# Kernel optimization log

Hardware: AMD Instinct MI355X
Metric: run time of the kernel (lower is better)

## Reference

```python
import jax, jax.numpy as jnp
import numpy as np

N_E = 1024
E_DIM = 256
BETA = 0.25
EPS_MASK = 1e-6
EPS_LOG = 1e-10


def setup_inputs() -> dict:
    key = jax.random.key(0)
    k1, k2, k3 = jax.random.split(key, 3)
    z = jax.random.normal(k1, (128, 512, E_DIM), dtype=jnp.float32)
    mask = jax.random.randint(k2, (128, 512), 0, 2, dtype=jnp.int32)
    emb_w = jax.random.uniform(k3, (N_E, E_DIM), dtype=jnp.float32,
                               minval=-1.0 / N_E, maxval=1.0 / N_E)
    return {"z": z, "mask": mask, "emb_w": emb_w}


def reference(z, mask, emb_w):
    sg = jax.lax.stop_gradient
    z_flat = z.reshape(-1, E_DIM)                       # (N, D)
    flat_mask = mask.reshape(-1, 1).astype(z.dtype)     # (N, 1)

    # squared euclidean distances: ||z||^2 + ||e||^2 - 2 z.e
    d = (jnp.sum(z_flat ** 2, axis=1, keepdims=True)
         + jnp.sum(emb_w ** 2, axis=1)
         - 2.0 * jnp.matmul(z_flat, emb_w.T))           # (N, n_e)
    idx = jnp.argmin(d, axis=1)                         # (N,)

    min_encodings = jax.nn.one_hot(idx, N_E, dtype=z.dtype)  # (N, n_e)
    # gather == one_hot @ emb_w, but without the redundant matmul
    z_q_flat = emb_w[idx]                               # (N, D)
    z_q = z_q_flat.reshape(z.shape)

    denom = jnp.sum(flat_mask) + EPS_MASK
    diff_c = (sg(z_q_flat) - z_flat) * flat_mask
    commitment_loss = jnp.sum(diff_c ** 2) / denom
    diff_e = (z_q_flat - sg(z_flat)) * flat_mask
    codebook_loss = jnp.sum(diff_e ** 2) / denom
    loss = commitment_loss + BETA * codebook_loss

    # straight-through estimator
    z_q_st = z + sg(z_q - z)

    e_mean = jnp.mean(min_encodings, axis=0)            # (n_e,)
    perplexity = jnp.exp(-jnp.sum(e_mean * jnp.log(e_mean + EPS_LOG)))

    return (loss, z_q_st, perplexity, min_encodings, idx[:, None])
```

## Files before the change

kernel.cpp:

```cpp
#include <hip/hip_runtime.h>
#include <stdint.h>
#include <stddef.h>

#define NROWS 65536
#define EDIM  256
#define NE    1024
#define CAP   24

static const long long OFF_ZQ   = 1LL;
static const long long OFF_PERP = 16777217LL;
static const long long OFF_ENC  = 16777218LL;
static const long long OFF_IDX  = 83886082LL;

typedef __attribute__((ext_vector_type(8))) short bf16x8;
typedef __attribute__((ext_vector_type(4))) float f32x4;

__device__ __forceinline__ unsigned short f2bf(float f) {
  unsigned u = __float_as_uint(f);
  return (unsigned short)((u + 0x7FFFu + ((u >> 16) & 1u)) >> 16);
}

__global__ __launch_bounds__(256) void k_emb(const float* __restrict__ emb,
                                             float* __restrict__ enorm,
                                             unsigned short* __restrict__ ebf16,
                                             unsigned int* __restrict__ hist,
                                             int* __restrict__ emaxbits) {
  if (blockIdx.x == 0) {
    for (int i = threadIdx.x; i < NE; i += 256) hist[i] = 0u;
  }
  int er   = blockIdx.x * 4 + (threadIdx.x >> 6);
  int lane = threadIdx.x & 63;
  float4 v = ((const float4*)(emb + (size_t)er * EDIM))[lane];
  ushort4 h;
  h.x = f2bf(v.x); h.y = f2bf(v.y); h.z = f2bf(v.z); h.w = f2bf(v.w);
  ((ushort4*)(ebf16 + (size_t)er * EDIM))[lane] = h;
  float s = v.x * v.x + v.y * v.y + v.z * v.z + v.w * v.w;
#pragma unroll
  for (int m = 1; m < 64; m <<= 1) s += __shfl_xor(s, m);
  if (lane == 0) {
    enorm[er] = s;
    atomicMax(emaxbits, (int)__float_as_uint(s));
  }
}

__global__ __launch_bounds__(256, 3) void k_main(
    const float* __restrict__ z, const float* __restrict__ emb,
    const unsigned short* __restrict__ ebf16,
    const float* __restrict__ enorm, const int* __restrict__ mask,
    const int* __restrict__ emaxbits,
    float* __restrict__ out, unsigned int* __restrict__ hist,
    float* __restrict__ Spart) {
  __shared__ unsigned short zb[32 * 264];
  __shared__ float en_s[NE];
  __shared__ float zn_s[32];
  __shared__ float wr_s[32];
  __shared__ unsigned int rmin_s[32];
  __shared__ unsigned short cand_s[32][CAP];
  __shared__ int ccnt_s[32];
  __shared__ float bestd_s[32][8];
  __shared__ int   besti_s[32][8];
  __shared__ int   idx_s[32];

  const int tid   = threadIdx.x;
  const int lane  = tid & 63;
  const int wid   = tid >> 6;
  const int l15   = lane & 15;
  const int l4    = lane >> 4;
  const int rbase = blockIdx.x * 32;

  {
    float4 zz = make_float4(0.f, 0.f, 0.f, 0.f);
    float4* encz = (float4*)(out + OFF_ENC + (size_t)rbase * NE);
#pragma unroll
    for (int j = 0; j < 8; ++j) encz[tid + j * 256] = zz;
  }

  if (tid < 32) { rmin_s[tid] = 0x7F800000u; ccnt_s[tid] = 0; }
  for (int i = tid; i < NE; i += 256) en_s[i] = enorm[i];

  {
#pragma unroll 1
    for (int rr = 0; rr < 8; ++rr) {
      int row_l = wid * 8 + rr;
      float4 v = ((const float4*)(z + (size_t)(rbase + row_l) * EDIM))[lane];
      float s = v.x * v.x + v.y * v.y + v.z * v.z + v.w * v.w;
#pragma unroll
      for (int m = 1; m < 64; m <<= 1) s += __shfl_xor(s, m);
      if (lane == 0) zn_s[row_l] = s;
      ushort4 h;
      h.x = f2bf(v.x); h.y = f2bf(v.y); h.z = f2bf(v.z); h.w = f2bf(v.w);
      ((ushort4*)&zb[row_l * 264])[lane] = h;
    }
  }
  __syncthreads();

  const float emaxf = __uint_as_float((unsigned)*emaxbits);
  if (tid < 32) wr_s[tid] = 0.025f * sqrtf(zn_s[tid] * emaxf) + 2.0e-4f;

  float znr[2][4];
#pragma unroll
  for (int rt = 0; rt < 2; ++rt)
#pragma unroll
    for (int reg = 0; reg < 4; ++reg) znr[rt][reg] = zn_s[rt * 16 + l4 * 4 + reg];

#pragma unroll 1
  for (int slab = 0; slab < 4; ++slab) {
    f32x4 acc[2][4];
#pragma unroll
    for (int rt = 0; rt < 2; ++rt)
#pragma unroll
      for (int ct = 0; ct < 4; ++ct) acc[rt][ct] = (f32x4){0.f, 0.f, 0.f, 0.f};

#pragma unroll 4
    for (int ch = 0; ch < 8; ++ch) {
      bf16x8 bv[4];
#pragma unroll
      for (int ct = 0; ct < 4; ++ct)
        bv[ct] = *(const bf16x8*)(ebf16
                    + (size_t)(slab * 256 + wid * 64 + ct * 16 + l15) * EDIM
                    + ch * 32 + l4 * 8);
      bf16x8 av0 = *(const bf16x8*)&zb[(0 * 16 + l15) * 264 + ch * 32 + l4 * 8];
      bf16x8 av1 = *(const bf16x8*)&zb[(1 * 16 + l15) * 264 + ch * 32 + l4 * 8];
#pragma unroll
      for (int ct = 0; ct < 4; ++ct) {
        acc[0][ct] = __builtin_amdgcn_mfma_f32_16x16x32_bf16(av0, bv[ct], acc[0][ct], 0, 0, 0);
        acc[1][ct] = __builtin_amdgcn_mfma_f32_16x16x32_bf16(av1, bv[ct], acc[1][ct], 0, 0, 0);
      }
    }

#pragma unroll
    for (int rt = 0; rt < 2; ++rt)
#pragma unroll
      for (int reg = 0; reg < 4; ++reg) {
        int row = rt * 16 + l4 * 4 + reg;
        float dm = 3.402823466e+38f;
#pragma unroll
        for (int ct = 0; ct < 4; ++ct) {
          int code = slab * 256 + wid * 64 + ct * 16 + l15;
          float t  = znr[rt][reg] + en_s[code];
          float dt = fmaf(-2.f, acc[rt][ct][reg], t);
          dm = fminf(dm, dt);
        }
#pragma unroll
        for (int m = 1; m < 16; m <<= 1) dm = fminf(dm, __shfl_xor(dm, m));
        if (l15 == 0) atomicMin(&rmin_s[row], __float_as_uint(dm));
      }
    __syncthreads();

#pragma unroll
    for (int rt = 0; rt < 2; ++rt)
#pragma unroll
      for (int reg = 0; reg < 4; ++reg) {
        int row = rt * 16 + l4 * 4 + reg;
        float thr = __uint_as_float(rmin_s[row]) + wr_s[row];
#pragma unroll
        for (int ct = 0; ct < 4; ++ct) {
          int code = slab * 256 + wid * 64 + ct * 16 + l15;
          float t  = znr[rt][reg] + en_s[code];
          float dt = fmaf(-2.f, acc[rt][ct][reg], t);
          if (dt <= thr) {
            int p = atomicAdd(&ccnt_s[row], 1);
            if (p < CAP) cand_s[row][p] = (unsigned short)code;
          }
        }
      }
  }
  __syncthreads();

  {
    const int sub  = tid >> 5;
    const int r    = tid & 31;
    const float* zp = z + (size_t)(rbase + r) * EDIM;
    float bd = 3.402823466e+38f;
    int   bi = 0x7FFFFFFF;
    int cnt = ccnt_s[r];
    if (cnt <= CAP) {
      for (int j = sub; j < cnt; j += 8) {
        int c = cand_s[r][j];
        const float* ep = emb + (size_t)c * EDIM;
        float p = 0.f;
#pragma unroll 8
        for (int k = 0; k < 256; ++k) p = fmaf(zp[k], ep[k], p);
        float t = zn_s[r] + en_s[c];
        float d = fmaf(-2.f, p, t);
        if (d < bd || (d == bd && c < bi)) { bd = d; bi = c; }
      }
    } else {
      for (int c = sub; c < NE; c += 8) {
        const float* ep = emb + (size_t)c * EDIM;
        float p = 0.f;
#pragma unroll 8
        for (int k = 0; k < 256; ++k) p = fmaf(zp[k], ep[k], p);
        float t = zn_s[r] + en_s[c];
        float d = fmaf(-2.f, p, t);
        if (d < bd || (d == bd && c < bi)) { bd = d; bi = c; }
      }
    }
    bestd_s[r][sub] = bd;
    besti_s[r][sub] = bi;
  }
  __syncthreads();
  if (tid < 32) {
    float bd = bestd_s[tid][0];
    int   bi = besti_s[tid][0];
#pragma unroll
    for (int j = 1; j < 8; ++j) {
      float od = bestd_s[tid][j];
      int   oi = besti_s[tid][j];
      if (od < bd || (od == bd && oi < bi)) { bd = od; bi = oi; }
    }
    idx_s[tid] = bi;
    out[(size_t)OFF_IDX + rbase + tid] = (float)bi;
  }
  __syncthreads();

#pragma unroll 1
  for (int rr = 0; rr < 8; ++rr) {
    int row_l = wid * 8 + rr;
    int row   = rbase + row_l;
    int idx   = idx_s[row_l];
    float4 zq = ((const float4*)(emb + (size_t)idx * EDIM))[lane];
    float4 zv = ((const float4*)(z + (size_t)row * EDIM))[lane];
    float4 st;
    st.x = zv.x + (zq.x - zv.x);
    st.y = zv.y + (zq.y - zv.y);
    st.z = zv.z + (zq.z - zv.z);
    st.w = zv.w + (zq.w - zv.w);
    ((float4*)(out + OFF_ZQ + (size_t)row * EDIM))[lane] = st;
    float m  = (float)mask[row];
    float dx = __fmul_rn(__fsub_rn(zq.x, zv.x), m);
    float dy = __fmul_rn(__fsub_rn(zq.y, zv.y), m);
    float dz = __fmul_rn(__fsub_rn(zq.z, zv.z), m);
    float dw = __fmul_rn(__fsub_rn(zq.w, zv.w), m);
    float px = __fmul_rn(dx, dx);
    float py = __fmul_rn(dy, dy);
    float pz = __fmul_rn(dz, dz);
    float pw = __fmul_rn(dw, dw);
    float p  = __fadd_rn(__fadd_rn(px, py), __fadd_rn(pz, pw));
#pragma unroll
    for (int s = 1; s < 64; s <<= 1) p = __fadd_rn(p, __shfl_xor(p, s));
    if (lane == 0) {
      Spart[row] = p;
      atomicAdd(&hist[idx], 1u);
      out[(size_t)OFF_ENC + (size_t)row * NE + idx] = 1.0f;
    }
  }
}

__global__ __launch_bounds__(1024) void k_final(const int* __restrict__ mask,
                                                const unsigned int* __restrict__ hist,
                                                const float* __restrict__ Spart,
                                                float* __restrict__ out) {
  int t = threadIdx.x;
  int ms = 0;
  for (int i = t; i < NROWS; i += 1024) ms += mask[i];
  double sp = 0.0;
  for (int i = t; i < NROWS; i += 1024) sp += (double)Spart[i];
  double ent = 0.0;
  {
    int i = t;
    float em = (float)hist[i] * (1.0f / 65536.0f);
    float lg = logf(em + 1e-10f);
    ent = (double)(em * lg);
  }
#pragma unroll
  for (int m = 1; m < 64; m <<= 1) {
    ms  += __shfl_xor(ms, m);
    sp  += __shfl_xor(sp, m);
    ent += __shfl_xor(ent, m);
  }
  __shared__ double redS[16], redE[16];
  __shared__ int    redM[16];
  int w = t >> 6;
  if ((t & 63) == 0) { redS[w] = sp; redE[w] = ent; redM[w] = ms; }
  __syncthreads();
  if (t == 0) {
    double S = 0.0, E = 0.0; int M = 0;
    for (int i = 0; i < 16; ++i) { S += redS[i]; E += redE[i]; M += redM[i]; }
    float denom = (float)M + 1e-6f;
    float Sf    = (float)S;
    float cl    = Sf / denom;
    out[0] = cl + 0.25f * cl;
    out[(size_t)OFF_PERP] = expf((float)(-E));
  }
}

extern "C" void kernel_launch(void* const* d_in, const int* in_sizes, int n_in,
                              void* d_out, int out_size, void* d_ws, size_t ws_size,
                              hipStream_t stream) {
  const float* z    = (const float*)d_in[0];
  const int*   mask = (const int*)d_in[1];
  const float* emb  = (const float*)d_in[2];
  float*       out  = (float*)d_out;

  float*          Spart    = (float*)d_ws;
  float*          enorm    = Spart + NROWS;
  unsigned int*   hist     = (unsigned int*)(enorm + NE);
  int*            emaxbits = (int*)(hist + NE);
  unsigned short* ebf16    = (unsigned short*)(emaxbits + 4);

  k_emb  <<<256,  256, 0, stream>>>(emb, enorm, ebf16, hist, emaxbits);
  k_main <<<2048, 256, 0, stream>>>(z, emb, ebf16, enorm, mask, emaxbits,
                                    out, hist, Spart);
  k_final<<<1,   1024, 0, stream>>>(mask, hist, Spart, out);
}
```

Measured before the change: 598.6 us.

## Use nontemporal output stores, software-pipeline MFMA loads, raise occupancy to 4

```diff
diff --git a/kernel.cpp b/kernel.cpp
--- a/kernel.cpp
+++ b/kernel.cpp
@@ -43,7 +43,7 @@
   }
 }
 
-__global__ __launch_bounds__(256, 3) void k_main(
+__global__ __launch_bounds__(256, 4) void k_main(
     const float* __restrict__ z, const float* __restrict__ emb,
     const unsigned short* __restrict__ ebf16,
     const float* __restrict__ enorm, const int* __restrict__ mask,
@@ -69,10 +69,11 @@
   const int rbase = blockIdx.x * 32;
 
   {
-    float4 zz = make_float4(0.f, 0.f, 0.f, 0.f);
-    float4* encz = (float4*)(out + OFF_ENC + (size_t)rbase * NE);
-#pragma unroll
-    for (int j = 0; j < 8; ++j) encz[tid + j * 256] = zz;
+    f32x4 zz = (f32x4){0.f, 0.f, 0.f, 0.f};
+    f32x4* encz = (f32x4*)(out + OFF_ENC + (size_t)rbase * NE);
+#pragma unroll
+    for (int j = 0; j < 8; ++j)
+      __builtin_nontemporal_store(zz, encz + tid + j * 256);
   }
 
   if (tid < 32) { rmin_s[tid] = 0x7F800000u; ccnt_s[tid] = 0; }
@@ -103,6 +104,9 @@
 #pragma unroll
     for (int reg = 0; reg < 4; ++reg) znr[rt][reg] = zn_s[rt * 16 + l4 * 4 + reg];
 
+  const unsigned short* pa0 = &zb[l15 * 264 + l4 * 8];
+  const unsigned short* pa1 = pa0 + 16 * 264;
+
 #pragma unroll 1
   for (int slab = 0; slab < 4; ++slab) {
     f32x4 acc[2][4];
@@ -111,22 +115,45 @@
 #pragma unroll
       for (int ct = 0; ct < 4; ++ct) acc[rt][ct] = (f32x4){0.f, 0.f, 0.f, 0.f};
 
-#pragma unroll 4
-    for (int ch = 0; ch < 8; ++ch) {
-      bf16x8 bv[4];
-#pragma unroll
-      for (int ct = 0; ct < 4; ++ct)
-        bv[ct] = *(const bf16x8*)(ebf16
-                    + (size_t)(slab * 256 + wid * 64 + ct * 16 + l15) * EDIM
-                    + ch * 32 + l4 * 8);
-      bf16x8 av0 = *(const bf16x8*)&zb[(0 * 16 + l15) * 264 + ch * 32 + l4 * 8];
-      bf16x8 av1 = *(const bf16x8*)&zb[(1 * 16 + l15) * 264 + ch * 32 + l4 * 8];
-#pragma unroll
-      for (int ct = 0; ct < 4; ++ct) {
-        acc[0][ct] = __builtin_amdgcn_mfma_f32_16x16x32_bf16(av0, bv[ct], acc[0][ct], 0, 0, 0);
-        acc[1][ct] = __builtin_amdgcn_mfma_f32_16x16x32_bf16(av1, bv[ct], acc[1][ct], 0, 0, 0);
-      }
-    }
+    const unsigned short* eb0 =
+        ebf16 + (size_t)(slab * 256 + wid * 64 + l15) * EDIM + l4 * 8;
+    const unsigned short* eb1 = eb0 + 16 * EDIM;
+    const unsigned short* eb2 = eb0 + 32 * EDIM;
+    const unsigned short* eb3 = eb0 + 48 * EDIM;
+
+    bf16x8 cb0 = *(const bf16x8*)(eb0);
+    bf16x8 cb1 = *(const bf16x8*)(eb1);
+    bf16x8 cb2 = *(const bf16x8*)(eb2);
+    bf16x8 cb3 = *(const bf16x8*)(eb3);
+    bf16x8 ca0 = *(const bf16x8*)(pa0);
+    bf16x8 ca1 = *(const bf16x8*)(pa1);
+
+#define MFMA8()                                                            \
+    acc[0][0] = __builtin_amdgcn_mfma_f32_16x16x32_bf16(ca0, cb0, acc[0][0], 0, 0, 0); \
+    acc[1][0] = __builtin_amdgcn_mfma_f32_16x16x32_bf16(ca1, cb0, acc[1][0], 0, 0, 0); \
+    acc[0][1] = __builtin_amdgcn_mfma_f32_16x16x32_bf16(ca0, cb1, acc[0][1], 0, 0, 0); \
+    acc[1][1] = __builtin_amdgcn_mfma_f32_16x16x32_bf16(ca1, cb1, acc[1][1], 0, 0, 0); \
+    acc[0][2] = __builtin_amdgcn_mfma_f32_16x16x32_bf16(ca0, cb2, acc[0][2], 0, 0, 0); \
+    acc[1][2] = __builtin_amdgcn_mfma_f32_16x16x32_bf16(ca1, cb2, acc[1][2], 0, 0, 0); \
+    acc[0][3] = __builtin_amdgcn_mfma_f32_16x16x32_bf16(ca0, cb3, acc[0][3], 0, 0, 0); \
+    acc[1][3] = __builtin_amdgcn_mfma_f32_16x16x32_bf16(ca1, cb3, acc[1][3], 0, 0, 0);
+
+#define STEP(ch)                                                           \
+    {                                                                      \
+      bf16x8 nb0 = *(const bf16x8*)(eb0 + ((ch) + 1) * 32);                \
+      bf16x8 nb1 = *(const bf16x8*)(eb1 + ((ch) + 1) * 32);                \
+      bf16x8 nb2 = *(const bf16x8*)(eb2 + ((ch) + 1) * 32);                \
+      bf16x8 nb3 = *(const bf16x8*)(eb3 + ((ch) + 1) * 32);                \
+      bf16x8 na0 = *(const bf16x8*)(pa0 + ((ch) + 1) * 32);                \
+      bf16x8 na1 = *(const bf16x8*)(pa1 + ((ch) + 1) * 32);                \
+      MFMA8();                                                             \
+      cb0 = nb0; cb1 = nb1; cb2 = nb2; cb3 = nb3; ca0 = na0; ca1 = na1;    \
+    }
+
+    STEP(0) STEP(1) STEP(2) STEP(3) STEP(4) STEP(5) STEP(6)
+    MFMA8();
+#undef STEP
+#undef MFMA8
 
 #pragma unroll
     for (int rt = 0; rt < 2; ++rt)
@@ -221,12 +248,12 @@
     int idx   = idx_s[row_l];
     float4 zq = ((const float4*)(emb + (size_t)idx * EDIM))[lane];
     float4 zv = ((const float4*)(z + (size_t)row * EDIM))[lane];
-    float4 st;
+    f32x4 st;
     st.x = zv.x + (zq.x - zv.x);
     st.y = zv.y + (zq.y - zv.y);
     st.z = zv.z + (zq.z - zv.z);
     st.w = zv.w + (zq.w - zv.w);
-    ((float4*)(out + OFF_ZQ + (size_t)row * EDIM))[lane] = st;
+    __builtin_nontemporal_store(st, (f32x4*)(out + OFF_ZQ + (size_t)row * EDIM) + lane);
     float m  = (float)mask[row];
     float dx = __fmul_rn(__fsub_rn(zq.x, zv.x), m);
     float dy = __fmul_rn(__fsub_rn(zq.y, zv.y), m);
```

New measurement: 594.5 us. About the same (-0.7%).
